# Kernel optimization log

Hardware: AMD Instinct MI355X
Metric: run time of the kernel (lower is better)

## Reference

```python
import jax, jax.numpy as jnp
import numpy as np

D_MODEL = 1024
N_HEADS = 16
D_K = D_MODEL // N_HEADS
B, L = 8, 512


def setup_inputs() -> dict:
    key = jax.random.key(0)
    ks = jax.random.split(key, 12)
    s = 0.02
    return {
        "q": jax.random.normal(ks[0], (B, L, D_MODEL), jnp.float32),
        "k": jax.random.normal(ks[1], (B, L, D_MODEL), jnp.float32),
        "v": jax.random.normal(ks[2], (B, L, D_MODEL), jnp.float32),
        "rel_pos_emb": jax.random.normal(ks[3], (L, L, D_MODEL), jnp.float32) * s,
        "mask": jnp.ones((1, 1, L, L), jnp.int32),
        "Wq": jax.random.normal(ks[4], (D_MODEL, D_MODEL), jnp.float32) * s,
        "bq": jnp.zeros((D_MODEL,), jnp.float32),
        "Wk": jax.random.normal(ks[5], (D_MODEL, D_MODEL), jnp.float32) * s,
        "bk": jnp.zeros((D_MODEL,), jnp.float32),
        "Wv": jax.random.normal(ks[6], (D_MODEL, D_MODEL), jnp.float32) * s,
        "bv": jnp.zeros((D_MODEL,), jnp.float32),
        "Wo": jax.random.normal(ks[7], (D_MODEL, D_MODEL), jnp.float32) * s,
        "bo": jnp.zeros((D_MODEL,), jnp.float32),
    }


def reference(q, k, v, rel_pos_emb, mask, Wq, bq, Wk, bk, Wv, bv, Wo, bo):
    Bn, Ln, D = q.shape
    H, dk = N_HEADS, D // N_HEADS
    # QKV projections (nn.Linear: x @ W^T + b), split heads -> [B,H,L,dk]
    qh = (q @ Wq.T + bq).reshape(Bn, Ln, H, dk).transpose(0, 2, 1, 3)
    kh = (k @ Wk.T + bk).reshape(Bn, Ln, H, dk).transpose(0, 2, 1, 3)
    vh = (v @ Wv.T + bv).reshape(Bn, Ln, H, dk).transpose(0, 2, 1, 3)
    # relative position embeddings -> [H,L,L,dk]
    rel = rel_pos_emb.reshape(Ln, Ln, H, dk).transpose(2, 0, 1, 3)
    scale = 1.0 / jnp.sqrt(jnp.float32(dk))
    scores = jnp.einsum('bhld,bhrd->bhlr', qh, kh) * scale
    scores = scores + jnp.einsum('bhld,hlrd->bhlr', qh, rel)
    scores = jnp.where(mask == 0, jnp.float32(-1e9), scores)
    attn = jax.nn.softmax(scores, axis=-1)  # dropout omitted (eval mode)
    out = jnp.einsum('bhlr,bhrd->bhld', attn, vh)
    out = out.transpose(0, 2, 1, 3).reshape(Bn, Ln, D)
    return out @ Wo.T + bo
```

## Files before the change

kernel.cpp:

```cpp
#include <hip/hip_runtime.h>

typedef __attribute__((ext_vector_type(8))) short short8;
typedef __attribute__((ext_vector_type(4))) float f32x4;
typedef __attribute__((ext_vector_type(4))) unsigned short u16x4;
typedef unsigned int u32;
typedef unsigned short ushort_t;

union frag_u { u32 w[4]; short8 s; };

static __device__ __forceinline__ unsigned short f2bf(float x) {
  union { float f; unsigned u; } v; v.f = x;
  unsigned r = v.u + 0x7fffu + ((v.u >> 16) & 1u);
  return (unsigned short)(r >> 16);
}
static __device__ __forceinline__ float bf2f(unsigned short h) {
  union { unsigned u; float f; } v; v.u = ((unsigned)h) << 16;
  return v.f;
}
static __device__ __forceinline__ u32 pk_bf16(float a, float b) {
  u32 r;
  asm("v_cvt_pk_bf16_f32 %0, %1, %2" : "=v"(r) : "v"(a), "v"(b));
  return r;
}

static __device__ __forceinline__ void barrier_lds() {
  __builtin_amdgcn_sched_barrier(0);
  asm volatile("s_waitcnt lgkmcnt(0)" ::: "memory");
  __builtin_amdgcn_s_barrier();
  __builtin_amdgcn_sched_barrier(0);
}
static __device__ __forceinline__ void barrier_plain() {
  __builtin_amdgcn_sched_barrier(0);
  __builtin_amdgcn_s_barrier();
  __builtin_amdgcn_sched_barrier(0);
}

static __device__ __forceinline__ void gl_lds16(const void* g, void* s) {
  __builtin_amdgcn_global_load_lds(
      (const __attribute__((address_space(1))) void*)g,
      (__attribute__((address_space(3))) void*)s, 16, 0, 0);
}

__global__ __launch_bounds__(256) void to_bf16_3(const float* __restrict__ s0,
                                                 const float* __restrict__ s1,
                                                 const float* __restrict__ s2,
                                                 ushort_t* __restrict__ dst,
                                                 int lg2, int n4) {
  int i = blockIdx.x * blockDim.x + threadIdx.x;
  int stride = gridDim.x * blockDim.x;
  for (; i < n4; i += stride) {
    int which = i >> lg2;
    const float* s = which == 0 ? s0 : which == 1 ? s1 : s2;
    int local = i - (which << lg2);
    float4 x = *(const float4*)&s[(size_t)local * 4];
    u16x4 o;
    o.x = f2bf(x.x); o.y = f2bf(x.y); o.z = f2bf(x.z); o.w = f2bf(x.w);
    *(u16x4*)&dst[(size_t)i * 4] = o;
  }
}

__global__ __launch_bounds__(256) void split3_bf16(const float* __restrict__ src,
                                                   ushort_t* __restrict__ dst, int n) {
  int i = blockIdx.x * blockDim.x + threadIdx.x;
  int stride = gridDim.x * blockDim.x;
  for (; i < n; i += stride) {
    int r = i >> 10, c = i & 1023;
    float x = src[i];
    unsigned short hi = f2bf(x);
    unsigned short lo = f2bf(x - bf2f(hi));
    ushort_t* row = dst + (size_t)r * 3072;
    row[c] = hi; row[1024 + c] = hi; row[2048 + c] = lo;
  }
}

__global__ __launch_bounds__(256) void gemm_qkv(
    const ushort_t* __restrict__ qbf, const ushort_t* __restrict__ kbf,
    const ushort_t* __restrict__ vbf, const ushort_t* __restrict__ Wqb,
    const ushort_t* __restrict__ Wkb, const ushort_t* __restrict__ Wvb,
    const float* __restrict__ bq, const float* __restrict__ bk,
    const float* __restrict__ bv, ushort_t* __restrict__ qhb,
    ushort_t* __restrict__ khb, ushort_t* __restrict__ vT) {
  __shared__ ushort_t As[2][128 * 32];
  __shared__ ushort_t Bs[2][128 * 32];
  const int t = threadIdx.x;
  const int lane = t & 63;
  const int w = t >> 6;
  const int wr = w >> 1, wc = w & 1;
  const int bid = blockIdx.x;
  const int mt = bid / 24, ntg = bid % 24;
  const int which = ntg >> 3, nt = ntg & 7;
  const ushort_t* A  = which == 0 ? qbf : which == 1 ? kbf : vbf;
  const ushort_t* Bw = which == 0 ? Wqb : which == 1 ? Wkb : Wvb;
  const float* bias  = which == 0 ? bq  : which == 1 ? bk  : bv;
  const int m0 = mt * 128, n0 = nt * 128;
  const int r16 = lane & 15, kb = lane >> 4;

  f32x4 acc[4][4];
#pragma unroll
  for (int mi = 0; mi < 4; ++mi)
#pragma unroll
    for (int ni = 0; ni < 4; ++ni) acc[mi][ni] = (f32x4){0.f, 0.f, 0.f, 0.f};

  auto STAGE = [&](int buf, int k0) {
#pragma unroll
    for (int i = 0; i < 2; ++i) {
      int c = i * 256 + t;
      int row = c >> 2, kc = (c & 3) * 8;
      gl_lds16(&A[(size_t)(m0 + row) * 1024 + k0 + kc], &As[buf][c * 8]);
      gl_lds16(&Bw[(size_t)(n0 + row) * 1024 + k0 + kc], &Bs[buf][c * 8]);
    }
  };

  STAGE(0, 0);
  __syncthreads();
  int cur = 0;
  for (int kt = 0; kt < 32; ++kt) {
    if (kt + 1 < 32) STAGE(cur ^ 1, (kt + 1) * 32);
    short8 af[4], bf[4];
#pragma unroll
    for (int mi = 0; mi < 4; ++mi)
      af[mi] = *(const short8*)&As[cur][(wr * 64 + mi * 16 + r16) * 32 + kb * 8];
#pragma unroll
    for (int ni = 0; ni < 4; ++ni)
      bf[ni] = *(const short8*)&Bs[cur][(wc * 64 + ni * 16 + r16) * 32 + kb * 8];
#pragma unroll
    for (int mi = 0; mi < 4; ++mi)
#pragma unroll
      for (int ni = 0; ni < 4; ++ni)
        acc[mi][ni] = __builtin_amdgcn_mfma_f32_16x16x32_bf16(af[mi], bf[ni], acc[mi][ni], 0, 0, 0);
    __syncthreads();
    cur ^= 1;
  }

  const int rowD = (lane >> 4) * 4;
#pragma unroll
  for (int mi = 0; mi < 4; ++mi) {
#pragma unroll
    for (int ni = 0; ni < 4; ++ni) {
      int n = n0 + wc * 64 + ni * 16 + (lane & 15);
      float bv4 = bias[n];
      int mbase = m0 + wr * 64 + mi * 16 + rowD;
      float vals[4];
#pragma unroll
      for (int j = 0; j < 4; ++j) vals[j] = acc[mi][ni][j] + bv4;
      int hh = n >> 6, d = n & 63;
      if (which == 0) {
#pragma unroll
        for (int j = 0; j < 4; ++j) {
          int m = mbase + j;
          int b = m >> 9, l = m & 511;
          qhb[(((size_t)(b * 16 + hh)) * 512 + l) * 64 + d] = f2bf(vals[j]);
        }
      } else if (which == 1) {
#pragma unroll
        for (int j = 0; j < 4; ++j) {
          int m = mbase + j;
          int b = m >> 9, r = m & 511;
          khb[(((size_t)(b * 16 + hh)) * 512 + r) * 64 + d] = f2bf(vals[j]);
        }
      } else {
        int b = mbase >> 9, r = mbase & 511;
        u16x4 pkv;
        pkv.x = f2bf(vals[0]); pkv.y = f2bf(vals[1]);
        pkv.z = f2bf(vals[2]); pkv.w = f2bf(vals[3]);
        *(u16x4*)&vT[(((size_t)(b * 16 + hh)) * 64 + d) * 512 + r] = pkv;
      }
    }
  }
}

__global__ __launch_bounds__(256) void gemm_out(const ushort_t* __restrict__ A,
                                                const ushort_t* __restrict__ Bw,
                                                const float* __restrict__ bias,
                                                float* __restrict__ Cout) {
  __shared__ ushort_t As[2][128 * 32];
  __shared__ ushort_t Bs[2][128 * 32];
  const int t = threadIdx.x;
  const int lane = t & 63;
  const int w = t >> 6;
  const int wr = w >> 1, wc = w & 1;
  const int mt = blockIdx.x >> 3, nt = blockIdx.x & 7;
  const int m0 = mt * 128, n0 = nt * 128;
  const int r16 = lane & 15, kb = lane >> 4;

  f32x4 acc[4][4];
#pragma unroll
  for (int mi = 0; mi < 4; ++mi)
#pragma unroll
    for (int ni = 0; ni < 4; ++ni) acc[mi][ni] = (f32x4){0.f, 0.f, 0.f, 0.f};

  auto STAGE = [&](int buf, int k0) {
#pragma unroll
    for (int i = 0; i < 2; ++i) {
      int c = i * 256 + t;
      int row = c >> 2, kc = (c & 3) * 8;
      gl_lds16(&A[(size_t)(m0 + row) * 3072 + k0 + kc], &As[buf][c * 8]);
      gl_lds16(&Bw[(size_t)(n0 + row) * 3072 + k0 + kc], &Bs[buf][c * 8]);
    }
  };

  STAGE(0, 0);
  __syncthreads();
  int cur = 0;
  for (int kt = 0; kt < 96; ++kt) {
    if (kt + 1 < 96) STAGE(cur ^ 1, (kt + 1) * 32);
    short8 af[4], bf[4];
#pragma unroll
    for (int mi = 0; mi < 4; ++mi)
      af[mi] = *(const short8*)&As[cur][(wr * 64 + mi * 16 + r16) * 32 + kb * 8];
#pragma unroll
    for (int ni = 0; ni < 4; ++ni)
      bf[ni] = *(const short8*)&Bs[cur][(wc * 64 + ni * 16 + r16) * 32 + kb * 8];
#pragma unroll
    for (int mi = 0; mi < 4; ++mi)
#pragma unroll
      for (int ni = 0; ni < 4; ++ni)
        acc[mi][ni] = __builtin_amdgcn_mfma_f32_16x16x32_bf16(af[mi], bf[ni], acc[mi][ni], 0, 0, 0);
    __syncthreads();
    cur ^= 1;
  }

  const int rowD = (lane >> 4) * 4;
#pragma unroll
  for (int mi = 0; mi < 4; ++mi) {
#pragma unroll
    for (int ni = 0; ni < 4; ++ni) {
      int n = n0 + wc * 64 + ni * 16 + (lane & 15);
      float bv = bias[n];
      int mbase = m0 + wr * 64 + mi * 16 + rowD;
#pragma unroll
      for (int j = 0; j < 4; ++j)
        Cout[(size_t)(mbase + j) * 1024 + n] = acc[mi][ni][j] + bv;
    }
  }
}

__global__ __launch_bounds__(256, 1) void attn_mfma(
    const ushort_t* __restrict__ qhb, const ushort_t* __restrict__ khb,
    const ushort_t* __restrict__ vT, const float* __restrict__ rel,
    const int* __restrict__ mask, ushort_t* __restrict__ Abig) {
  __shared__ float relL[2][16][16][64];
  __shared__ ushort_t qs[8][16][64];
  __shared__ float sp2[8][17][20];
  const int t = threadIdx.x;
  const int w = t >> 6, lane = t & 63, lh = lane & 15, lg = lane >> 4;
  const int w4 = w * 4;
  const int bid = blockIdx.x;
  const int slot = bid & 7, grp = bid >> 3;
  const int h = slot * 2 + (grp & 1);
  const int l0 = (grp >> 1) * 16;
  const int b0 = w * 2;
  const int off = (grp * 5) & 31;

  {
    int idx = t * 32;
    int b = idx >> 10, l = (idx >> 6) & 15, d0 = idx & 63;
    const ushort_t* src = &qhb[(((size_t)(b * 16 + h)) * 512 + l0 + l) * 64 + d0];
    int xr = (l & 7) ^ b;
#pragma unroll
    for (int jj = 0; jj < 4; ++jj) {
      short8 vq = *(const short8*)&src[jj * 8];
      int pos = ((d0 >> 3) + jj) ^ xr;
      *(short8*)&qs[b][l][pos * 8] = vq;
    }
  }

  const int rdel = lane >> 4;
  const int blk = lane & 15;
  auto DMA_REL = [&](int buf, int r0_) {
#pragma unroll
    for (int j = 0; j < 16; ++j) {
      const int li = j >> 2;
      const int rr4 = (j & 3) * 4;
      const int r_local = rr4 + rdel;
      const int blkp = blk ^ (r_local & 7);
      const float* src = rel +
          ((size_t)(l0 + w4 + li) * 512 + r0_ + r_local) * 1024 + h * 64 + blkp * 4;
      gl_lds16(src, &relL[buf][w4 + li][rr4][0]);
    }
  };

  f32x4 O[2][4];
#pragma unroll
  for (int i = 0; i < 2; ++i)
#pragma unroll
    for (int j = 0; j < 4; ++j) O[i][j] = (f32x4){0.f, 0.f, 0.f, 0.f};
  float m_run[2] = {-1e30f, -1e30f}, s_run[2] = {0.f, 0.f};

  __syncthreads();
  DMA_REL(0, off * 16);

#pragma unroll 1
  for (int it = 0; it < 32; ++it) {
    const int r0 = ((it + off) & 31) * 16;
    const int cur = it & 1;

    short8 kf[2][2], vf[2][4];
#pragma unroll
    for (int bh = 0; bh < 2; ++bh) {
#pragma unroll
      for (int kb = 0; kb < 2; ++kb)
        kf[bh][kb] = *(const short8*)&khb[(((size_t)((b0 + bh) * 16 + h)) * 512 + r0 + lh) * 64 + kb * 32 + lg * 8];
#pragma unroll
      for (int dt = 0; dt < 4; ++dt)
        vf[bh][dt] = *(const short8*)&vT[(((size_t)((b0 + bh) * 16 + h)) * 64 + dt * 16 + lh) * 512 + r0 + lg * 8];
    }
    int4 mk = *(const int4*)&mask[(size_t)(l0 + lh) * 512 + r0 + lg * 4];

    __builtin_amdgcn_sched_barrier(0);
    DMA_REL(cur ^ 1, (((it + 1 + off) & 31)) * 16);
    __builtin_amdgcn_sched_barrier(0);
    asm volatile("s_waitcnt vmcnt(16)" ::: "memory");
    __builtin_amdgcn_sched_barrier(0);

#pragma unroll
    for (int li = 0; li < 4; ++li) {
      const int l = w4 + li;
      const float* row = &relL[cur][l][lh][0];
      const int s = lh & 7;
      frag_u a0, a1;
      {
        int bb = lg * 2;
        f32x4 Ra = *(const f32x4*)(row + ((bb ^ s) * 4));
        f32x4 Rb = *(const f32x4*)(row + (((bb + 1) ^ s) * 4));
        a0.w[0] = pk_bf16(Ra[0], Ra[1]); a0.w[1] = pk_bf16(Ra[2], Ra[3]);
        a0.w[2] = pk_bf16(Rb[0], Rb[1]); a0.w[3] = pk_bf16(Rb[2], Rb[3]);
      }
      {
        int bb = 8 + lg * 2;
        f32x4 Ra = *(const f32x4*)(row + ((bb ^ s) * 4));
        f32x4 Rb = *(const f32x4*)(row + (((bb + 1) ^ s) * 4));
        a1.w[0] = pk_bf16(Ra[0], Ra[1]); a1.w[1] = pk_bf16(Ra[2], Ra[3]);
        a1.w[2] = pk_bf16(Rb[0], Rb[1]); a1.w[3] = pk_bf16(Rb[2], Rb[3]);
      }
      int xr2 = (l & 7) ^ (lh & 7);
      short8 q0 = *(const short8*)&qs[lh & 7][l][(lg ^ xr2) * 8];
      short8 q1 = *(const short8*)&qs[lh & 7][l][((4 + lg) ^ xr2) * 8];
      f32x4 acc = (f32x4){0.f, 0.f, 0.f, 0.f};
      acc = __builtin_amdgcn_mfma_f32_16x16x32_bf16(a0.s, q0, acc, 0, 0, 0);
      acc = __builtin_amdgcn_mfma_f32_16x16x32_bf16(a1.s, q1, acc, 0, 0, 0);
      if (lh < 8) *(f32x4*)&sp2[lh][l][lg * 4] = acc;
    }

    barrier_lds();

    __builtin_amdgcn_s_setprio(1);
#pragma unroll
    for (int bh = 0; bh < 2; ++bh) {
      int xqk = (lh & 7) ^ (b0 + bh);
      short8 qb0 = *(const short8*)&qs[b0 + bh][lh][(lg ^ xqk) * 8];
      short8 qb1 = *(const short8*)&qs[b0 + bh][lh][((4 + lg) ^ xqk) * 8];
      f32x4 s1 = (f32x4){0.f, 0.f, 0.f, 0.f};
      s1 = __builtin_amdgcn_mfma_f32_16x16x32_bf16(kf[bh][0], qb0, s1, 0, 0, 0);
      s1 = __builtin_amdgcn_mfma_f32_16x16x32_bf16(kf[bh][1], qb1, s1, 0, 0, 0);
      f32x4 s2 = *(const f32x4*)&sp2[b0 + bh][lh][lg * 4];
      f32x4 S;
      S[0] = (mk.x == 0) ? -1e9f : (s1[0] * 0.125f + s2[0]);
      S[1] = (mk.y == 0) ? -1e9f : (s1[1] * 0.125f + s2[1]);
      S[2] = (mk.z == 0) ? -1e9f : (s1[2] * 0.125f + s2[2]);
      S[3] = (mk.w == 0) ? -1e9f : (s1[3] * 0.125f + s2[3]);
      float mt = fmaxf(fmaxf(S[0], S[1]), fmaxf(S[2], S[3]));
      mt = fmaxf(mt, __shfl_xor(mt, 16));
      mt = fmaxf(mt, __shfl_xor(mt, 32));
      float mn = fmaxf(m_run[bh], mt);
      float fsc = __expf(m_run[bh] - mn);
      f32x4 P;
      P[0] = __expf(S[0] - mn); P[1] = __expf(S[1] - mn);
      P[2] = __expf(S[2] - mn); P[3] = __expf(S[3] - mn);
      float ps = P[0] + P[1] + P[2] + P[3];
      ps += __shfl_xor(ps, 16);
      ps += __shfl_xor(ps, 32);
      s_run[bh] = s_run[bh] * fsc + ps;
      m_run[bh] = mn;
#pragma unroll
      for (int dt = 0; dt < 4; ++dt) O[bh][dt] *= fsc;
      u32 pk0 = pk_bf16(P[0], P[1]), pk1 = pk_bf16(P[2], P[3]);
      int s0l = (lh + 32 * lg) & 63;
      u32 w0 = (u32)__shfl((int)pk0, s0l), w1 = (u32)__shfl((int)pk1, s0l);
      u32 w2 = (u32)__shfl((int)pk0, s0l + 16), w3 = (u32)__shfl((int)pk1, s0l + 16);
      bool vld = (lg < 2);
      frag_u pb;
      pb.w[0] = vld ? w0 : 0u; pb.w[1] = vld ? w1 : 0u;
      pb.w[2] = vld ? w2 : 0u; pb.w[3] = vld ? w3 : 0u;
#pragma unroll
      for (int dt = 0; dt < 4; ++dt)
        O[bh][dt] = __builtin_amdgcn_mfma_f32_16x16x32_bf16(vf[bh][dt], pb.s, O[bh][dt], 0, 0, 0);
    }
    __builtin_amdgcn_s_setprio(0);

    barrier_plain();
  }

#pragma unroll
  for (int bh = 0; bh < 2; ++bh) {
    float inv = 1.0f / s_run[bh];
    ushort_t* rowp = &Abig[(size_t)((b0 + bh) * 512 + l0 + lh) * 3072];
#pragma unroll
    for (int dt = 0; dt < 4; ++dt) {
      int c = h * 64 + dt * 16 + lg * 4;
      f32x4 o = O[bh][dt];
      float x0 = o[0] * inv, x1 = o[1] * inv, x2 = o[2] * inv, x3 = o[3] * inv;
      u16x4 hi, lo;
      hi.x = f2bf(x0); lo.x = f2bf(x0 - bf2f(hi.x));
      hi.y = f2bf(x1); lo.y = f2bf(x1 - bf2f(hi.y));
      hi.z = f2bf(x2); lo.z = f2bf(x2 - bf2f(hi.z));
      hi.w = f2bf(x3); lo.w = f2bf(x3 - bf2f(hi.w));
      *(u16x4*)&rowp[c] = hi;
      *(u16x4*)&rowp[1024 + c] = lo;
      *(u16x4*)&rowp[2048 + c] = hi;
    }
  }
}

extern "C" void kernel_launch(void* const* d_in, const int* in_sizes, int n_in,
                              void* d_out, int out_size, void* d_ws, size_t ws_size,
                              hipStream_t stream) {
  const float* q    = (const float*)d_in[0];
  const float* k    = (const float*)d_in[1];
  const float* v    = (const float*)d_in[2];
  const float* rel  = (const float*)d_in[3];
  const int*   mask = (const int*)d_in[4];
  const float* Wq   = (const float*)d_in[5];
  const float* bq   = (const float*)d_in[6];
  const float* Wk   = (const float*)d_in[7];
  const float* bk   = (const float*)d_in[8];
  const float* Wv   = (const float*)d_in[9];
  const float* bv   = (const float*)d_in[10];
  const float* Wo   = (const float*)d_in[11];
  const float* bo   = (const float*)d_in[12];
  float* out = (float*)d_out;

  char* ws = (char*)d_ws;
  ushort_t* qhb = (ushort_t*)(ws);
  ushort_t* khb = (ushort_t*)(ws + 16777216);
  ushort_t* vT  = (ushort_t*)(ws + 16777216 + 8388608);
  ushort_t* X   = (ushort_t*)(ws + 33554432);
  ushort_t* Y   = (ushort_t*)(ws + 58720256);
  ushort_t* qbf = X;
  ushort_t* kbf = X + 4194304;
  ushort_t* vbf = X + 8388608;
  ushort_t* Wqb = Y;
  ushort_t* Wkb = Y + 1048576;
  ushort_t* Wvb = Y + 2097152;

  to_bf16_3<<<1536, 256, 0, stream>>>(q, k, v, X, 20, 3145728);
  to_bf16_3<<<384, 256, 0, stream>>>(Wq, Wk, Wv, Y, 18, 786432);

  gemm_qkv<<<768, 256, 0, stream>>>(qbf, kbf, vbf, Wqb, Wkb, Wvb,
                                    bq, bk, bv, qhb, khb, vT);

  split3_bf16<<<1024, 256, 0, stream>>>(Wo, Y, 1048576);

  attn_mfma<<<512, 256, 0, stream>>>(qhb, khb, vT, rel, mask, X);

  gemm_out<<<256, 256, 0, stream>>>(X, Y, bo, out);
}
```

Before: 481.4 us.

## Halve attention key tile, keep Q in registers, double-buffer sp2 to drop barrier

The attention kernel now processes 8 key positions per iteration instead of 16, which halves the LDS staging buffer for rel_pos_emb. Q fragments are loaded once into registers instead of going through a swizzled LDS tile. The sp2 score buffer is double-buffered so the trailing per-iteration barrier can be removed, and launch bounds request two blocks per CU to raise occupancy. The cost is twice as many loop iterations and half-wasted MFMA lanes: 16-wide tiles carry only 8 valid key rows, and invalid rows are masked to -1e9. There is also more register pressure from holding Q fragments.

```diff
diff --git a/kernel.cpp b/kernel.cpp
--- a/kernel.cpp
+++ b/kernel.cpp
@@ -26,11 +26,6 @@
 static __device__ __forceinline__ void barrier_lds() {
   __builtin_amdgcn_sched_barrier(0);
   asm volatile("s_waitcnt lgkmcnt(0)" ::: "memory");
-  __builtin_amdgcn_s_barrier();
-  __builtin_amdgcn_sched_barrier(0);
-}
-static __device__ __forceinline__ void barrier_plain() {
-  __builtin_amdgcn_sched_barrier(0);
   __builtin_amdgcn_s_barrier();
   __builtin_amdgcn_sched_barrier(0);
 }
@@ -235,13 +230,12 @@
   }
 }
 
-__global__ __launch_bounds__(256, 1) void attn_mfma(
+__global__ __launch_bounds__(256, 2) void attn_mfma(
     const ushort_t* __restrict__ qhb, const ushort_t* __restrict__ khb,
     const ushort_t* __restrict__ vT, const float* __restrict__ rel,
     const int* __restrict__ mask, ushort_t* __restrict__ Abig) {
-  __shared__ float relL[2][16][16][64];
-  __shared__ ushort_t qs[8][16][64];
-  __shared__ float sp2[8][17][20];
+  __shared__ float relL[2][16][8][64];
+  __shared__ float sp2[2][8][17][12];
   const int t = threadIdx.x;
   const int w = t >> 6, lane = t & 63, lh = lane & 15, lg = lane >> 4;
   const int w4 = w * 4;
@@ -250,32 +244,34 @@
   const int h = slot * 2 + (grp & 1);
   const int l0 = (grp >> 1) * 16;
   const int b0 = w * 2;
-  const int off = (grp * 5) & 31;
-
-  {
-    int idx = t * 32;
-    int b = idx >> 10, l = (idx >> 6) & 15, d0 = idx & 63;
-    const ushort_t* src = &qhb[(((size_t)(b * 16 + h)) * 512 + l0 + l) * 64 + d0];
-    int xr = (l & 7) ^ b;
-#pragma unroll
-    for (int jj = 0; jj < 4; ++jj) {
-      short8 vq = *(const short8*)&src[jj * 8];
-      int pos = ((d0 >> 3) + jj) ^ xr;
-      *(short8*)&qs[b][l][pos * 8] = vq;
-    }
+  const int off = (grp * 21) & 63;
+
+  short8 qb0[2], qb1[2];
+#pragma unroll
+  for (int bh = 0; bh < 2; ++bh) {
+    const ushort_t* qp = &qhb[(((size_t)((b0 + bh) * 16 + h)) * 512 + l0 + lh) * 64 + lg * 8];
+    qb0[bh] = *(const short8*)qp;
+    qb1[bh] = *(const short8*)(qp + 32);
+  }
+  short8 q0f[4], q1f[4];
+#pragma unroll
+  for (int li = 0; li < 4; ++li) {
+    const ushort_t* qp = &qhb[(((size_t)((lh & 7) * 16 + h)) * 512 + l0 + w4 + li) * 64 + lg * 8];
+    q0f[li] = *(const short8*)qp;
+    q1f[li] = *(const short8*)(qp + 32);
   }
 
   const int rdel = lane >> 4;
   const int blk = lane & 15;
   auto DMA_REL = [&](int buf, int r0_) {
 #pragma unroll
-    for (int j = 0; j < 16; ++j) {
-      const int li = j >> 2;
-      const int rr4 = (j & 3) * 4;
-      const int r_local = rr4 + rdel;
-      const int blkp = blk ^ (r_local & 7);
+    for (int j = 0; j < 8; ++j) {
+      const int li = j >> 1;
+      const int rr4 = (j & 1) * 4;
+      const int rl = rr4 + rdel;
+      const int blkp = blk ^ rl;
       const float* src = rel +
-          ((size_t)(l0 + w4 + li) * 512 + r0_ + r_local) * 1024 + h * 64 + blkp * 4;
+          ((size_t)(l0 + w4 + li) * 512 + r0_ + rl) * 1024 + h * 64 + blkp * 4;
       gl_lds16(src, &relL[buf][w4 + li][rr4][0]);
     }
   };
@@ -287,36 +283,35 @@
     for (int j = 0; j < 4; ++j) O[i][j] = (f32x4){0.f, 0.f, 0.f, 0.f};
   float m_run[2] = {-1e30f, -1e30f}, s_run[2] = {0.f, 0.f};
 
-  __syncthreads();
-  DMA_REL(0, off * 16);
+  DMA_REL(0, (off & 63) * 8);
 
 #pragma unroll 1
-  for (int it = 0; it < 32; ++it) {
-    const int r0 = ((it + off) & 31) * 16;
+  for (int it = 0; it < 64; ++it) {
+    const int r0 = ((it + off) & 63) * 8;
     const int cur = it & 1;
 
+    __builtin_amdgcn_sched_barrier(0);
+    DMA_REL(cur ^ 1, (((it + 1 + off) & 63)) * 8);
+    __builtin_amdgcn_sched_barrier(0);
+    asm volatile("s_waitcnt vmcnt(8)" ::: "memory");
+    __builtin_amdgcn_sched_barrier(0);
+
     short8 kf[2][2], vf[2][4];
 #pragma unroll
     for (int bh = 0; bh < 2; ++bh) {
 #pragma unroll
       for (int kb = 0; kb < 2; ++kb)
-        kf[bh][kb] = *(const short8*)&khb[(((size_t)((b0 + bh) * 16 + h)) * 512 + r0 + lh) * 64 + kb * 32 + lg * 8];
+        kf[bh][kb] = *(const short8*)&khb[(((size_t)((b0 + bh) * 16 + h)) * 512 + r0 + (lh & 7)) * 64 + kb * 32 + lg * 8];
 #pragma unroll
       for (int dt = 0; dt < 4; ++dt)
         vf[bh][dt] = *(const short8*)&vT[(((size_t)((b0 + bh) * 16 + h)) * 64 + dt * 16 + lh) * 512 + r0 + lg * 8];
     }
-    int4 mk = *(const int4*)&mask[(size_t)(l0 + lh) * 512 + r0 + lg * 4];
-
-    __builtin_amdgcn_sched_barrier(0);
-    DMA_REL(cur ^ 1, (((it + 1 + off) & 31)) * 16);
-    __builtin_amdgcn_sched_barrier(0);
-    asm volatile("s_waitcnt vmcnt(16)" ::: "memory");
-    __builtin_amdgcn_sched_barrier(0);
+    int4 mk = *(const int4*)&mask[(size_t)(l0 + lh) * 512 + r0 + (lg & 1) * 4];
 
 #pragma unroll
     for (int li = 0; li < 4; ++li) {
       const int l = w4 + li;
-      const float* row = &relL[cur][l][lh][0];
+      const float* row = &relL[cur][l][lh & 7][0];
       const int s = lh & 7;
       frag_u a0, a1;
       {
@@ -333,32 +328,27 @@
         a1.w[0] = pk_bf16(Ra[0], Ra[1]); a1.w[1] = pk_bf16(Ra[2], Ra[3]);
         a1.w[2] = pk_bf16(Rb[0], Rb[1]); a1.w[3] = pk_bf16(Rb[2], Rb[3]);
       }
-      int xr2 = (l & 7) ^ (lh & 7);
-      short8 q0 = *(const short8*)&qs[lh & 7][l][(lg ^ xr2) * 8];
-      short8 q1 = *(const short8*)&qs[lh & 7][l][((4 + lg) ^ xr2) * 8];
       f32x4 acc = (f32x4){0.f, 0.f, 0.f, 0.f};
-      acc = __builtin_amdgcn_mfma_f32_16x16x32_bf16(a0.s, q0, acc, 0, 0, 0);
-      acc = __builtin_amdgcn_mfma_f32_16x16x32_bf16(a1.s, q1, acc, 0, 0, 0);
-      if (lh < 8) *(f32x4*)&sp2[lh][l][lg * 4] = acc;
+      acc = __builtin_amdgcn_mfma_f32_16x16x32_bf16(a0.s, q0f[li], acc, 0, 0, 0);
+      acc = __builtin_amdgcn_mfma_f32_16x16x32_bf16(a1.s, q1f[li], acc, 0, 0, 0);
+      if (lh < 8 && lg < 2) *(f32x4*)&sp2[cur][lh][l][lg * 4] = acc;
     }
 
     barrier_lds();
 
     __builtin_amdgcn_s_setprio(1);
+    const bool vrow = (lg < 2);
 #pragma unroll
     for (int bh = 0; bh < 2; ++bh) {
-      int xqk = (lh & 7) ^ (b0 + bh);
-      short8 qb0 = *(const short8*)&qs[b0 + bh][lh][(lg ^ xqk) * 8];
-      short8 qb1 = *(const short8*)&qs[b0 + bh][lh][((4 + lg) ^ xqk) * 8];
       f32x4 s1 = (f32x4){0.f, 0.f, 0.f, 0.f};
-      s1 = __builtin_amdgcn_mfma_f32_16x16x32_bf16(kf[bh][0], qb0, s1, 0, 0, 0);
-      s1 = __builtin_amdgcn_mfma_f32_16x16x32_bf16(kf[bh][1], qb1, s1, 0, 0, 0);
-      f32x4 s2 = *(const f32x4*)&sp2[b0 + bh][lh][lg * 4];
+      s1 = __builtin_amdgcn_mfma_f32_16x16x32_bf16(kf[bh][0], qb0[bh], s1, 0, 0, 0);
+      s1 = __builtin_amdgcn_mfma_f32_16x16x32_bf16(kf[bh][1], qb1[bh], s1, 0, 0, 0);
+      f32x4 s2 = *(const f32x4*)&sp2[cur][b0 + bh][lh][lg * 4];
       f32x4 S;
-      S[0] = (mk.x == 0) ? -1e9f : (s1[0] * 0.125f + s2[0]);
-      S[1] = (mk.y == 0) ? -1e9f : (s1[1] * 0.125f + s2[1]);
-      S[2] = (mk.z == 0) ? -1e9f : (s1[2] * 0.125f + s2[2]);
-      S[3] = (mk.w == 0) ? -1e9f : (s1[3] * 0.125f + s2[3]);
+      S[0] = (vrow && mk.x != 0) ? (s1[0] * 0.125f + s2[0]) : -1e9f;
+      S[1] = (vrow && mk.y != 0) ? (s1[1] * 0.125f + s2[1]) : -1e9f;
+      S[2] = (vrow && mk.z != 0) ? (s1[2] * 0.125f + s2[2]) : -1e9f;
+      S[3] = (vrow && mk.w != 0) ? (s1[3] * 0.125f + s2[3]) : -1e9f;
       float mt = fmaxf(fmaxf(S[0], S[1]), fmaxf(S[2], S[3]));
       mt = fmaxf(mt, __shfl_xor(mt, 16));
       mt = fmaxf(mt, __shfl_xor(mt, 32));
@@ -387,8 +377,6 @@
         O[bh][dt] = __builtin_amdgcn_mfma_f32_16x16x32_bf16(vf[bh][dt], pb.s, O[bh][dt], 0, 0, 0);
     }
     __builtin_amdgcn_s_setprio(0);
-
-    barrier_plain();
   }
 
 #pragma unroll
```

Result: slower. 541.4 us (+12.5%).
